# Kernel optimization log

Measured on AMD Instinct MI355X. Metric: run time of the kernel, lower is better.

Reference implementation:

```python
import jax, jax.numpy as jnp
import numpy as np

EPS = 1e-6  # floor

def setup_inputs() -> dict:
    key = jax.random.key(0)
    k1, = jax.random.split(key, 1)
    # mel-spectrogram magnitudes: non-negative
    x = jax.random.uniform(k1, (64, 2048, 160, 1), dtype=jnp.float32)  # [B,T,F,C]
    alpha = jnp.array([0.98], dtype=jnp.float32)
    smooth = jnp.array([0.03], dtype=jnp.float32)
    delta = jnp.array([2.0], dtype=jnp.float32)
    root = jnp.array([0.5], dtype=jnp.float32)
    return {"x": x, "alpha": alpha, "smooth": smooth, "delta": delta, "root": root}

def reference(x, alpha, smooth, delta, root):
    # EMA recurrence over time: m[t] = (1 - s) * x[t] + s * m[t-1], m[-1] = 0
    xt = jnp.swapaxes(x, 0, 1)  # [T,B,F,C]

    def step(prev, cur):
        new = (1.0 - smooth) * cur + smooth * prev
        return new, new

    _, smoothed_t = jax.lax.scan(step, jnp.zeros_like(xt[0]), xt)
    smoothed = jnp.swapaxes(smoothed_t, 0, 1)  # [B,T,F,C]

    # PCEN: (x / (eps + M)^alpha + delta)^root - delta^root
    pcen = (x / (EPS + smoothed) ** alpha + delta) ** root - delta ** root
    return pcen
```

## Files before the change

kernel.cpp:

```cpp
#include <hip/hip_runtime.h>
#include <stdint.h>

#define EPS 1e-6f

constexpr int Bq   = 64;
constexpr int Tq   = 2048;
constexpr int Fq   = 160;
constexpr int FQ4  = 40;
constexpr int ROWS = 64;
constexpr int WARM = 8;
constexpr int CH   = 8;
constexpr int TPB  = 320;
constexpr int NTILE = Tq / ROWS;
constexpr int TILE_ROWS  = ROWS + WARM;
constexpr int TILE_BYTES = TILE_ROWS * Fq * 4;
constexpr int MAIN_BYTES = ROWS * Fq * 4;

typedef float f4 __attribute__((ext_vector_type(4)));

__device__ __forceinline__ float fast_pow_pos(float b, float e) {
    return __builtin_amdgcn_exp2f(e * __builtin_amdgcn_logf(b));
}

__device__ __forceinline__ float pcen_one(float xv, float m, float na, float r,
                                          float d, float droot) {
    float ratio = xv * __builtin_amdgcn_exp2f(na * __builtin_amdgcn_logf(EPS + m));
    return fast_pow_pos(ratio + d, r) - droot;
}

__device__ __forceinline__ void load_lds_16(const void* g, void* l) {
    __builtin_amdgcn_global_load_lds(
        (const unsigned int __attribute__((address_space(1)))*)(uintptr_t)g,
        (unsigned int __attribute__((address_space(3)))*)(uint32_t)(uintptr_t)l,
        16, 0, 0);
}

__global__ __launch_bounds__(TPB) void pcen_kernel(
    const float* __restrict__ x,
    const float* __restrict__ alpha_p,
    const float* __restrict__ smooth_p,
    const float* __restrict__ delta_p,
    const float* __restrict__ root_p,
    float* __restrict__ out)
{
    __shared__ __align__(16) float lds[TILE_ROWS * Fq];

    const int tile  = blockIdx.x % NTILE;
    const int b     = blockIdx.x / NTILE;
    const int r0    = b * Tq + tile * ROWS;
    const bool first = (tile == 0);

    const int wave = threadIdx.x >> 6;
    const int lane = threadIdx.x & 63;

    {
        const char* src = (const char*)(x + (size_t)(first ? r0 : r0 - WARM) * Fq);
        char*       dst = (char*)lds + (first ? WARM * Fq * 4 : 0);
        const int   per = (first ? MAIN_BYTES : TILE_BYTES) / 1024 / 5;
        for (int i = 0; i < per; ++i) {
            const int off = (wave + 5 * i) * 1024;
            load_lds_16(src + off + lane * 16, dst + off);
        }
    }

    const float s     = smooth_p[0];
    const float a     = alpha_p[0];
    const float d     = delta_p[0];
    const float r     = root_p[0];
    const float oms   = 1.0f - s;
    const float na    = -a;
    const float droot = fast_pow_pos(d, r);

    __syncthreads();

    const int f = threadIdx.x % FQ4;
    const int c = threadIdx.x / FQ4;

    f4 m = (f4){0.f, 0.f, 0.f, 0.f};

    if (!(first && c == 0)) {
#pragma unroll
        for (int j = 0; j < WARM; ++j) {
            f4 xv = *(const f4*)&lds[(c * CH + j) * Fq + f * 4];
            m.x = fmaf(s, m.x, oms * xv.x);
            m.y = fmaf(s, m.y, oms * xv.y);
            m.z = fmaf(s, m.z, oms * xv.z);
            m.w = fmaf(s, m.w, oms * xv.w);
        }
    }

    f4* __restrict__ outr = (f4*)out;
    const int gbase = (r0 + c * CH) * FQ4 + f;

#pragma unroll
    for (int j = 0; j < CH; ++j) {
        f4 xv = *(const f4*)&lds[(WARM + c * CH + j) * Fq + f * 4];
        m.x = fmaf(s, m.x, oms * xv.x);
        m.y = fmaf(s, m.y, oms * xv.y);
        m.z = fmaf(s, m.z, oms * xv.z);
        m.w = fmaf(s, m.w, oms * xv.w);
        f4 o;
        o.x = pcen_one(xv.x, m.x, na, r, d, droot);
        o.y = pcen_one(xv.y, m.y, na, r, d, droot);
        o.z = pcen_one(xv.z, m.z, na, r, d, droot);
        o.w = pcen_one(xv.w, m.w, na, r, d, droot);
        __builtin_nontemporal_store(o, &outr[gbase + j * FQ4]);
    }
}

extern "C" void kernel_launch(void* const* d_in, const int* in_sizes, int n_in,
                              void* d_out, int out_size, void* d_ws, size_t ws_size,
                              hipStream_t stream) {
    const float* x      = (const float*)d_in[0];
    const float* alpha  = (const float*)d_in[1];
    const float* smooth = (const float*)d_in[2];
    const float* delta  = (const float*)d_in[3];
    const float* root   = (const float*)d_in[4];
    float* out          = (float*)d_out;

    const int blocks = Bq * NTILE;

    pcen_kernel<<<blocks, TPB, 0, stream>>>(x, alpha, smooth, delta, root, out);
}
```

Before: 156.5 us.

## Add sqrt fast path for root 0.5, factor EMA scale, remap workgroups across XCDs

Adds a runtime specialization: when root equals 0.5 the outer power becomes a single hardware sqrt instead of a log/exp2 pair. The EMA is kept unscaled, with (1-s) folded into the eps FMA, which removes a multiply per element. Workgroup IDs are also remapped so consecutive tiles land on the same XCD (8-way interleave), which may change L2 locality. The kernel is likely memory-bound, so the ALU savings may matter little.

```diff
diff --git a/kernel.cpp b/kernel.cpp
--- a/kernel.cpp
+++ b/kernel.cpp
@@ -12,6 +12,7 @@
 constexpr int CH   = 8;
 constexpr int TPB  = 320;
 constexpr int NTILE = Tq / ROWS;
+constexpr int NWG   = Bq * NTILE;
 constexpr int TILE_ROWS  = ROWS + WARM;
 constexpr int TILE_BYTES = TILE_ROWS * Fq * 4;
 constexpr int MAIN_BYTES = ROWS * Fq * 4;
@@ -22,10 +23,13 @@
     return __builtin_amdgcn_exp2f(e * __builtin_amdgcn_logf(b));
 }
 
-__device__ __forceinline__ float pcen_one(float xv, float m, float na, float r,
-                                          float d, float droot) {
-    float ratio = xv * __builtin_amdgcn_exp2f(na * __builtin_amdgcn_logf(EPS + m));
-    return fast_pow_pos(ratio + d, r) - droot;
+template<bool RSQ>
+__device__ __forceinline__ float pcen_one(float xv, float h, float na, float oms,
+                                          float r, float d, float droot) {
+    float me    = fmaf(oms, h, EPS);
+    float ratio = xv * __builtin_amdgcn_exp2f(na * __builtin_amdgcn_logf(me));
+    if (RSQ) return __builtin_amdgcn_sqrtf(ratio + d) - droot;
+    else     return fast_pow_pos(ratio + d, r) - droot;
 }
 
 __device__ __forceinline__ void load_lds_16(const void* g, void* l) {
@@ -33,6 +37,28 @@
         (const unsigned int __attribute__((address_space(1)))*)(uintptr_t)g,
         (unsigned int __attribute__((address_space(3)))*)(uint32_t)(uintptr_t)l,
         16, 0, 0);
+}
+
+template<bool RSQ>
+__device__ __forceinline__ void main_loop(const float* __restrict__ lds,
+                                          int c, int f, f4 h,
+                                          float s, float oms, float na,
+                                          float r, float d, float droot,
+                                          f4* __restrict__ outr, int gbase) {
+#pragma unroll
+    for (int j = 0; j < CH; ++j) {
+        f4 xv = *(const f4*)&lds[(WARM + c * CH + j) * Fq + f * 4];
+        h.x = fmaf(s, h.x, xv.x);
+        h.y = fmaf(s, h.y, xv.y);
+        h.z = fmaf(s, h.z, xv.z);
+        h.w = fmaf(s, h.w, xv.w);
+        f4 o;
+        o.x = pcen_one<RSQ>(xv.x, h.x, na, oms, r, d, droot);
+        o.y = pcen_one<RSQ>(xv.y, h.y, na, oms, r, d, droot);
+        o.z = pcen_one<RSQ>(xv.z, h.z, na, oms, r, d, droot);
+        o.w = pcen_one<RSQ>(xv.w, h.w, na, oms, r, d, droot);
+        __builtin_nontemporal_store(o, &outr[gbase + j * FQ4]);
+    }
 }
 
 __global__ __launch_bounds__(TPB) void pcen_kernel(
@@ -45,8 +71,9 @@
 {
     __shared__ __align__(16) float lds[TILE_ROWS * Fq];
 
-    const int tile  = blockIdx.x % NTILE;
-    const int b     = blockIdx.x / NTILE;
+    const int wg    = ((blockIdx.x & 7) << 8) | (blockIdx.x >> 3);
+    const int tile  = wg % NTILE;
+    const int b     = wg / NTILE;
     const int r0    = b * Tq + tile * ROWS;
     const bool first = (tile == 0);
 
@@ -69,43 +96,32 @@
     const float r     = root_p[0];
     const float oms   = 1.0f - s;
     const float na    = -a;
-    const float droot = fast_pow_pos(d, r);
+    const bool  rsq   = (r == 0.5f);
+    const float droot = rsq ? __builtin_amdgcn_sqrtf(d) : fast_pow_pos(d, r);
 
     __syncthreads();
 
     const int f = threadIdx.x % FQ4;
     const int c = threadIdx.x / FQ4;
 
-    f4 m = (f4){0.f, 0.f, 0.f, 0.f};
+    f4 h = (f4){0.f, 0.f, 0.f, 0.f};
 
     if (!(first && c == 0)) {
 #pragma unroll
         for (int j = 0; j < WARM; ++j) {
             f4 xv = *(const f4*)&lds[(c * CH + j) * Fq + f * 4];
-            m.x = fmaf(s, m.x, oms * xv.x);
-            m.y = fmaf(s, m.y, oms * xv.y);
-            m.z = fmaf(s, m.z, oms * xv.z);
-            m.w = fmaf(s, m.w, oms * xv.w);
+            h.x = fmaf(s, h.x, xv.x);
+            h.y = fmaf(s, h.y, xv.y);
+            h.z = fmaf(s, h.z, xv.z);
+            h.w = fmaf(s, h.w, xv.w);
         }
     }
 
     f4* __restrict__ outr = (f4*)out;
     const int gbase = (r0 + c * CH) * FQ4 + f;
 
-#pragma unroll
-    for (int j = 0; j < CH; ++j) {
-        f4 xv = *(const f4*)&lds[(WARM + c * CH + j) * Fq + f * 4];
-        m.x = fmaf(s, m.x, oms * xv.x);
-        m.y = fmaf(s, m.y, oms * xv.y);
-        m.z = fmaf(s, m.z, oms * xv.z);
-        m.w = fmaf(s, m.w, oms * xv.w);
-        f4 o;
-        o.x = pcen_one(xv.x, m.x, na, r, d, droot);
-        o.y = pcen_one(xv.y, m.y, na, r, d, droot);
-        o.z = pcen_one(xv.z, m.z, na, r, d, droot);
-        o.w = pcen_one(xv.w, m.w, na, r, d, droot);
-        __builtin_nontemporal_store(o, &outr[gbase + j * FQ4]);
-    }
+    if (rsq) main_loop<true >(lds, c, f, h, s, oms, na, r, d, droot, outr, gbase);
+    else     main_loop<false>(lds, c, f, h, s, oms, na, r, d, droot, outr, gbase);
 }
 
 extern "C" void kernel_launch(void* const* d_in, const int* in_sizes, int n_in,
@@ -118,7 +134,5 @@
     const float* root   = (const float*)d_in[4];
     float* out          = (float*)d_out;
 
-    const int blocks = Bq * NTILE;
-
-    pcen_kernel<<<blocks, TPB, 0, stream>>>(x, alpha, smooth, delta, root, out);
+    pcen_kernel<<<NWG, TPB, 0, stream>>>(x, alpha, smooth, delta, root, out);
 }
```

Result: no change. 156.8 us (+0.2%).
